# Kernel tuning notes

Measured on AMD Instinct MI355X. Metric: run time of the kernel, lower is better.

## Reference

```python
import jax, jax.numpy as jnp
import numpy as np

N = 50000   # nodes
E = 600000  # edges
H = 128     # hidden_dim


def _linear_params(key, fan_in, fan_out):
    kw, kb = jax.random.split(key)
    s = 1.0 / np.sqrt(fan_in)
    w = jax.random.uniform(kw, (fan_in, fan_out), minval=-s, maxval=s, dtype=jnp.float32)
    b = jax.random.uniform(kb, (fan_out,), minval=-s, maxval=s, dtype=jnp.float32)
    return w, b


def setup_inputs():
    key = jax.random.key(0)
    ks = jax.random.split(key, 9)
    x = jax.random.uniform(ks[0], (N, 1), dtype=jnp.float32)
    pre_h = jax.random.normal(ks[1], (N, H), dtype=jnp.float32)
    edge_index = jax.random.randint(ks[2], (2, E), 0, N, dtype=jnp.int32)
    edge_attr = jax.random.uniform(ks[3], (E, 1), dtype=jnp.float32)
    enc_w, enc_b = _linear_params(ks[4], 1 + H, H)      # BFS_Encoder.linear
    M_w, M_b = _linear_params(ks[5], H + H + 1, H)      # MPNN_Processor.M
    U_w, U_b = _linear_params(ks[6], H + H, H)          # MPNN_Processor.U
    dec_w, dec_b = _linear_params(ks[7], H + H, 1)      # BFS_Decoder.linear
    ter_w, ter_b = _linear_params(ks[8], H + H, 1)      # BFS_Terminator.linear
    return {"x": x, "pre_h": pre_h, "edge_attr": edge_attr,
            "enc_w": enc_w, "enc_b": enc_b, "M_w": M_w, "M_b": M_b,
            "U_w": U_w, "U_b": U_b, "dec_w": dec_w, "dec_b": dec_b,
            "ter_w": ter_w, "ter_b": ter_b, "edge_index": edge_index}


def reference(x, pre_h, edge_attr, enc_w, enc_b, M_w, M_b, U_w, U_b,
              dec_w, dec_b, ter_w, ter_b, edge_index):
    # Encoder: z = relu(Linear([x, pre_h]))
    z = jax.nn.relu(jnp.concatenate([x, pre_h], axis=-1) @ enc_w + enc_b)  # [N,H]

    # Processor (PyG MessagePassing, flow source_to_target):
    # z_i = z[edge_index[1]] (target), z_j = z[edge_index[0]] (source)
    src, tgt = edge_index[0], edge_index[1]
    m = jax.nn.relu(
        jnp.concatenate([z[tgt], z[src], edge_attr], axis=-1) @ M_w + M_b)  # [E,H]
    # scatter-max aggregate into target nodes; empty segments -> 0
    agg = jax.ops.segment_max(m, tgt, num_segments=N)
    agg = jnp.where(jnp.isfinite(agg), agg, 0.0)
    h = jax.nn.relu(jnp.concatenate([z, agg], axis=-1) @ U_w + U_b)  # [N,H]

    # Decoder
    y = jax.nn.sigmoid(jnp.concatenate([z, h], axis=-1) @ dec_w + dec_b)  # [N,1]

    # Terminator: mean over nodes, broadcast-concat, scalar mean
    h_mean = jnp.broadcast_to(jnp.mean(h, axis=0), h.shape)
    ter = jnp.mean(jnp.concatenate([h, h_mean], axis=-1) @ ter_w + ter_b)
    return h, y, ter
```

## Files before the change

### kernel.cpp

```cpp
#include <hip/hip_runtime.h>
#include <hip/hip_bf16.h>
#include <math.h>

#define HD 128
#define APAD 136

typedef short bf16x8 __attribute__((ext_vector_type(8)));
typedef float f32x4 __attribute__((ext_vector_type(4)));

static __device__ __forceinline__ unsigned short f2bf(float f) {
  __hip_bfloat16 b = __float2bfloat16(f);
  return *(unsigned short*)&b;
}
static __device__ __forceinline__ float bflo(unsigned int u) {
  return __uint_as_float(u << 16);
}
static __device__ __forceinline__ float bfhi(unsigned int u) {
  return __uint_as_float(u & 0xffff0000u);
}

__global__ __launch_bounds__(256) void k_frag_hist(
    const float* __restrict__ enc_w, const float* __restrict__ M_w,
    const float* __restrict__ U_w,
    unsigned short* __restrict__ encf, unsigned short* __restrict__ Pf,
    unsigned short* __restrict__ Qf, unsigned short* __restrict__ Uf,
    const int* __restrict__ ei, int* __restrict__ cnt, int E) {
  const int b = blockIdx.x;
  if (b >= 40) {
    const int e = (b - 40) * 256 + threadIdx.x;
    if (e < E) atomicAdd(&cnt[ei[E + e]], 1);
    return;
  }
  const float* W; unsigned short* F; int KS; int lb;
  if (b < 8)       { W = enc_w + HD;     F = encf; KS = 4; lb = b; }
  else if (b < 16) { W = M_w;            F = Pf;   KS = 4; lb = b - 8; }
  else if (b < 24) { W = M_w + HD * HD;  F = Qf;   KS = 4; lb = b - 16; }
  else             { W = U_w;            F = Uf;   KS = 8; lb = b - 24; }
  const int gid = lb * 256 + threadIdx.x;
  const int lane = gid & 63;
  const int ks = (gid >> 6) % KS;
  const int tile = gid / (64 * KS);
  const int col = tile * 16 + (lane & 15);
  const int k0 = ks * 32 + (lane >> 4) * 8;
  unsigned short v[8];
#pragma unroll
  for (int j = 0; j < 8; ++j) v[j] = f2bf(W[(size_t)(k0 + j) * HD + col]);
  unsigned short* dst = F + ((size_t)(tile * KS + ks) * 64 + lane) * 8;
#pragma unroll
  for (int j = 0; j < 8; ++j) dst[j] = v[j];
}

__global__ __launch_bounds__(256) void k_scan_block(
    const int* __restrict__ cnt, int* __restrict__ row_ptr,
    int* __restrict__ partials, int N) {
  __shared__ int s[256];
  const int t = threadIdx.x;
  const int base = blockIdx.x * 1024 + t * 4;
  int v[4], sum = 0;
#pragma unroll
  for (int i = 0; i < 4; ++i) {
    v[i] = (base + i < N) ? cnt[base + i] : 0;
    sum += v[i];
  }
  s[t] = sum;
  __syncthreads();
  for (int off = 1; off < 256; off <<= 1) {
    int xv = (t >= off) ? s[t - off] : 0;
    __syncthreads();
    if (t >= off) s[t] += xv;
    __syncthreads();
  }
  int run = s[t] - sum;
  if (t == 255) partials[blockIdx.x] = s[255];
#pragma unroll
  for (int i = 0; i < 4; ++i) {
    if (base + i < N) row_ptr[base + i] = run;
    run += v[i];
  }
}

__global__ void k_scan_partials(int* __restrict__ partials, int nb) {
  if (threadIdx.x == 0) {
    int run = 0;
    for (int i = 0; i < nb; ++i) { int v = partials[i]; partials[i] = run; run += v; }
  }
}

__global__ __launch_bounds__(256) void k_scan_add(
    int* __restrict__ row_ptr, const int* __restrict__ partials,
    int* __restrict__ cursor, int N) {
  const int base = blockIdx.x * 1024 + threadIdx.x * 4;
  const int p = partials[blockIdx.x];
#pragma unroll
  for (int i = 0; i < 4; ++i) {
    if (base + i < N) {
      int v = row_ptr[base + i] + p;
      row_ptr[base + i] = v;
      cursor[base + i] = v;
    }
  }
}

__global__ __launch_bounds__(256) void k_scatter(
    const int* __restrict__ ei, const float* __restrict__ edge_attr,
    int* __restrict__ cursor, int2* __restrict__ epack, int E) {
  const int e = blockIdx.x * 256 + threadIdx.x;
  if (e >= E) return;
  const int tgt = ei[E + e];
  const int pos = atomicAdd(&cursor[tgt], 1);
  epack[pos] = make_int2(ei[e], __float_as_int(edge_attr[e]));
}

__global__ __launch_bounds__(256, 4) void k_enc_pq(
    const float* __restrict__ x, const float* __restrict__ pre_h,
    const float* __restrict__ enc_w, const float* __restrict__ enc_b,
    const float* __restrict__ M_b,
    const unsigned short* __restrict__ encf, const unsigned short* __restrict__ Pf,
    const unsigned short* __restrict__ Qf,
    unsigned short* __restrict__ zg, unsigned short* __restrict__ Pg,
    unsigned short* __restrict__ Qg) {
  __shared__ unsigned short phs[16 * APAD];
  __shared__ unsigned short zsh[16 * APAD];
  __shared__ float xs[16];
  const int t = threadIdx.x;
  const int n0 = blockIdx.x * 16;

  {
    const int r = t >> 4, c0 = (t & 15) * 8;
    const float4 a = *(const float4*)&pre_h[(size_t)(n0 + r) * HD + c0];
    const float4 b = *(const float4*)&pre_h[(size_t)(n0 + r) * HD + c0 + 4];
    unsigned short* d = &phs[r * APAD + c0];
    d[0] = f2bf(a.x); d[1] = f2bf(a.y); d[2] = f2bf(a.z); d[3] = f2bf(a.w);
    d[4] = f2bf(b.x); d[5] = f2bf(b.y); d[6] = f2bf(b.z); d[7] = f2bf(b.w);
  }
  if (t < 16) xs[t] = x[n0 + t];
  __syncthreads();

  const int w = t >> 6, l = t & 63;
  const int m = l & 15, q = l >> 4;

  bf16x8 af[4];
#pragma unroll
  for (int ks = 0; ks < 4; ++ks)
    af[ks] = *(const bf16x8*)&phs[m * APAD + ks * 32 + q * 8];
  f32x4 acc[2] = {{0, 0, 0, 0}, {0, 0, 0, 0}};
#pragma unroll
  for (int tt = 0; tt < 2; ++tt) {
    const int tn = 2 * w + tt;
#pragma unroll
    for (int ks = 0; ks < 4; ++ks) {
      const bf16x8 bf = *(const bf16x8*)&encf[((size_t)(tn * 4 + ks) * 64 + l) * 8];
      acc[tt] = __builtin_amdgcn_mfma_f32_16x16x32_bf16(af[ks], bf, acc[tt], 0, 0, 0);
    }
  }
#pragma unroll
  for (int tt = 0; tt < 2; ++tt) {
    const int col = (2 * w + tt) * 16 + m;
    const float bb = enc_b[col];
    const float w0 = enc_w[col];
#pragma unroll
    for (int r = 0; r < 4; ++r) {
      const int row = q * 4 + r;
      const float zv = fmaxf(acc[tt][r] + bb + xs[row] * w0, 0.0f);
      zsh[row * APAD + col] = f2bf(zv);
    }
  }
  __syncthreads();

  bf16x8 az[4];
#pragma unroll
  for (int ks = 0; ks < 4; ++ks)
    az[ks] = *(const bf16x8*)&zsh[m * APAD + ks * 32 + q * 8];
  {
    const int r = t >> 4, c0 = (t & 15) * 8;
    *(uint4*)&zg[(size_t)(n0 + r) * HD + c0] = *(const uint4*)&zsh[r * APAD + c0];
  }
  __syncthreads();

  f32x4 pacc[2] = {{0, 0, 0, 0}, {0, 0, 0, 0}};
  f32x4 qacc[2] = {{0, 0, 0, 0}, {0, 0, 0, 0}};
#pragma unroll
  for (int tt = 0; tt < 2; ++tt) {
    const int tn = 2 * w + tt;
#pragma unroll
    for (int ks = 0; ks < 4; ++ks) {
      const bf16x8 bp = *(const bf16x8*)&Pf[((size_t)(tn * 4 + ks) * 64 + l) * 8];
      const bf16x8 bq = *(const bf16x8*)&Qf[((size_t)(tn * 4 + ks) * 64 + l) * 8];
      pacc[tt] = __builtin_amdgcn_mfma_f32_16x16x32_bf16(az[ks], bp, pacc[tt], 0, 0, 0);
      qacc[tt] = __builtin_amdgcn_mfma_f32_16x16x32_bf16(az[ks], bq, qacc[tt], 0, 0, 0);
    }
  }
#pragma unroll
  for (int tt = 0; tt < 2; ++tt) {
    const int col = (2 * w + tt) * 16 + m;
    const float mb = M_b[col];
#pragma unroll
    for (int r = 0; r < 4; ++r) {
      const int row = q * 4 + r;
      phs[row * APAD + col] = f2bf(pacc[tt][r] + mb);
      zsh[row * APAD + col] = f2bf(qacc[tt][r]);
    }
  }
  __syncthreads();
  {
    const int r = t >> 4, c0 = (t & 15) * 8;
    *(uint4*)&Pg[(size_t)(n0 + r) * HD + c0] = *(const uint4*)&phs[r * APAD + c0];
    *(uint4*)&Qg[(size_t)(n0 + r) * HD + c0] = *(const uint4*)&zsh[r * APAD + c0];
  }
}

__global__ __launch_bounds__(256, 6) void k_gather(
    const unsigned short* __restrict__ Pg, const unsigned short* __restrict__ Qg,
    const float* __restrict__ w_attr,
    const int* __restrict__ row_ptr, const int* __restrict__ row_end,
    const int2* __restrict__ epack,
    unsigned short* __restrict__ ag, int N) {
  const int t = threadIdx.x;
  const int w = t >> 6, l = t & 63;
  const int g = l >> 4, j = l & 15;
  const int n0 = blockIdx.x * 32;

  float wv[8];
  {
    const float4 wa = *(const float4*)&w_attr[j * 8];
    const float4 wb = *(const float4*)&w_attr[j * 8 + 4];
    wv[0] = wa.x; wv[1] = wa.y; wv[2] = wa.z; wv[3] = wa.w;
    wv[4] = wb.x; wv[5] = wb.y; wv[6] = wb.z; wv[7] = wb.w;
  }

#pragma unroll
  for (int i = 0; i < 2; ++i) {
    const int r = w * 8 + g * 2 + i;
    const int n = n0 + r;
    const int nc = min(n, N - 1);
    const int rs = row_ptr[nc], re = row_end[nc];
    float acc[8];
#pragma unroll
    for (int c = 0; c < 8; ++c) acc[c] = -INFINITY;
    for (int e = rs; e < re; e += 4) {
      int2 pk[4];
#pragma unroll
      for (int u = 0; u < 4; ++u) pk[u] = epack[min(e + u, re - 1)];
      uint4 qv[4];
#pragma unroll
      for (int u = 0; u < 4; ++u)
        qv[u] = *(const uint4*)&Qg[(size_t)pk[u].x * HD + j * 8];
#pragma unroll
      for (int u = 0; u < 4; ++u) {
        const float a = __int_as_float(pk[u].y);
        const unsigned int qq[4] = {qv[u].x, qv[u].y, qv[u].z, qv[u].w};
#pragma unroll
        for (int c = 0; c < 4; ++c) {
          acc[2 * c]     = fmaxf(acc[2 * c],     fmaf(a, wv[2 * c],     bflo(qq[c])));
          acc[2 * c + 1] = fmaxf(acc[2 * c + 1], fmaf(a, wv[2 * c + 1], bfhi(qq[c])));
        }
      }
    }
    if (n < N) {
      float res[8];
      if (re > rs) {
        const uint4 pv = *(const uint4*)&Pg[(size_t)n * HD + j * 8];
        const unsigned int pp[4] = {pv.x, pv.y, pv.z, pv.w};
#pragma unroll
        for (int c = 0; c < 4; ++c) {
          res[2 * c]     = fmaxf(bflo(pp[c]) + acc[2 * c],     0.0f);
          res[2 * c + 1] = fmaxf(bfhi(pp[c]) + acc[2 * c + 1], 0.0f);
        }
      } else {
#pragma unroll
        for (int c = 0; c < 8; ++c) res[c] = 0.0f;
      }
      uint4 st;
      st.x = (unsigned)f2bf(res[0]) | ((unsigned)f2bf(res[1]) << 16);
      st.y = (unsigned)f2bf(res[2]) | ((unsigned)f2bf(res[3]) << 16);
      st.z = (unsigned)f2bf(res[4]) | ((unsigned)f2bf(res[5]) << 16);
      st.w = (unsigned)f2bf(res[6]) | ((unsigned)f2bf(res[7]) << 16);
      *(uint4*)&ag[(size_t)n * HD + j * 8] = st;
    }
  }
}

__global__ __launch_bounds__(256, 4) void k_update(
    const unsigned short* __restrict__ zg, const unsigned short* __restrict__ ag,
    const unsigned short* __restrict__ Uf,
    const float* __restrict__ U_b, const float* __restrict__ dec_w,
    const float* __restrict__ dec_b,
    float* __restrict__ h_out, float* __restrict__ y_out,
    float* __restrict__ hsum, int N) {
  __shared__ unsigned short zsh[32 * APAD];
  __shared__ unsigned short ash[32 * APAD];
  __shared__ float hcol[HD];
  __shared__ float dacc[32];
  __shared__ float pr[32][8];
  const int t = threadIdx.x;
  const int n0 = blockIdx.x * 32;

  {
    const int r = t >> 3, c0 = (t & 7) * 16;
    const int n = min(n0 + r, N - 1);
    *(uint4*)&zsh[r * APAD + c0]     = *(const uint4*)&zg[(size_t)n * HD + c0];
    *(uint4*)&zsh[r * APAD + c0 + 8] = *(const uint4*)&zg[(size_t)n * HD + c0 + 8];
    *(uint4*)&ash[r * APAD + c0]     = *(const uint4*)&ag[(size_t)n * HD + c0];
    *(uint4*)&ash[r * APAD + c0 + 8] = *(const uint4*)&ag[(size_t)n * HD + c0 + 8];
  }
  if (t < 32) dacc[t] = 0.0f;
  if (t < HD) hcol[t] = 0.0f;
  __syncthreads();

  const int w = t >> 6, l = t & 63;

  const int mt = w & 1, nh = w >> 1;
  const int m = mt * 16 + (l & 15), q = l >> 4;
  bf16x8 afz[4], afa[4];
#pragma unroll
  for (int ks = 0; ks < 4; ++ks) {
    afz[ks] = *(const bf16x8*)&zsh[m * APAD + ks * 32 + q * 8];
    afa[ks] = *(const bf16x8*)&ash[m * APAD + ks * 32 + q * 8];
  }
  f32x4 acc4[4] = {{0, 0, 0, 0}, {0, 0, 0, 0}, {0, 0, 0, 0}, {0, 0, 0, 0}};
#pragma unroll
  for (int tt = 0; tt < 4; ++tt) {
    const int tn = nh * 4 + tt;
#pragma unroll
    for (int ks = 0; ks < 8; ++ks) {
      const bf16x8 bf = *(const bf16x8*)&Uf[((size_t)(tn * 8 + ks) * 64 + l) * 8];
      const bf16x8 a = (ks < 4) ? afz[ks] : afa[ks - 4];
      acc4[tt] = __builtin_amdgcn_mfma_f32_16x16x32_bf16(a, bf, acc4[tt], 0, 0, 0);
    }
  }
  float dp[4] = {0.0f, 0.0f, 0.0f, 0.0f};
#pragma unroll
  for (int tt = 0; tt < 4; ++tt) {
    const int col = (nh * 4 + tt) * 16 + (l & 15);
    const float ub = U_b[col];
    const float dw = dec_w[HD + col];
    float s4 = 0.0f;
#pragma unroll
    for (int r = 0; r < 4; ++r) {
      const int rowl = mt * 16 + q * 4 + r;
      const int n = n0 + rowl;
      float hv = fmaxf(acc4[tt][r] + ub, 0.0f);
      if (n < N) h_out[(size_t)n * HD + col] = hv; else hv = 0.0f;
      s4 += hv;
      dp[r] += hv * dw;
    }
    atomicAdd(&hcol[col], s4);
  }
#pragma unroll
  for (int off = 1; off < 16; off <<= 1) {
#pragma unroll
    for (int r = 0; r < 4; ++r) dp[r] += __shfl_xor(dp[r], off);
  }
  if ((l & 15) == 0) {
#pragma unroll
    for (int r = 0; r < 4; ++r) atomicAdd(&dacc[mt * 16 + q * 4 + r], dp[r]);
  }

  {
    const int r2 = t >> 3, s = t & 7;
    float part = 0.0f;
#pragma unroll
    for (int c = 0; c < 8; ++c) {
      const int kk = s * 16 + 2 * c;
      const unsigned int zu = *(const unsigned int*)&zsh[r2 * APAD + kk];
      part += bflo(zu) * dec_w[kk] + bfhi(zu) * dec_w[kk + 1];
    }
    pr[r2][s] = part;
  }
  __syncthreads();

  if (t < HD) atomicAdd(&hsum[t], hcol[t]);
  if (t < 32 && n0 + t < N) {
    float d = dec_b[0] + dacc[t];
#pragma unroll
    for (int s = 0; s < 8; ++s) d += pr[t][s];
    y_out[n0 + t] = 1.0f / (1.0f + expf(-d));
  }
}

__global__ __launch_bounds__(128) void k_ter(
    const float* __restrict__ hsum, const float* __restrict__ ter_w,
    const float* __restrict__ ter_b, float* __restrict__ out, float invN) {
  __shared__ float r2[2];
  const int t = threadIdx.x;
  float v = (hsum[t] * invN) * (ter_w[t] + ter_w[HD + t]);
#pragma unroll
  for (int o = 32; o > 0; o >>= 1) v += __shfl_down(v, o);
  if ((t & 63) == 0) r2[t >> 6] = v;
  __syncthreads();
  if (t == 0) out[0] = r2[0] + r2[1] + ter_b[0];
}

extern "C" void kernel_launch(void* const* d_in, const int* in_sizes, int n_in,
                              void* d_out, int out_size, void* d_ws, size_t ws_size,
                              hipStream_t stream) {
  const float* x        = (const float*)d_in[0];
  const float* pre_h    = (const float*)d_in[1];
  const float* edge_attr= (const float*)d_in[2];
  const float* enc_w    = (const float*)d_in[3];
  const float* enc_b    = (const float*)d_in[4];
  const float* M_w      = (const float*)d_in[5];
  const float* M_b      = (const float*)d_in[6];
  const float* U_w      = (const float*)d_in[7];
  const float* U_b      = (const float*)d_in[8];
  const float* dec_w    = (const float*)d_in[9];
  const float* dec_b    = (const float*)d_in[10];
  const float* ter_w    = (const float*)d_in[11];
  const float* ter_b    = (const float*)d_in[12];
  const int*   edge_idx = (const int*)d_in[13];

  const int N = in_sizes[0];
  const int E = in_sizes[2];
  const size_t NH = (size_t)N * HD;

  float* out = (float*)d_out;
  float* h_out = out;
  float* y_out = out + NH;
  float* ter_out = out + NH + N;

  unsigned short* zg = (unsigned short*)d_ws;
  unsigned short* Pg = zg + NH;
  unsigned short* Qg = Pg + NH;
  unsigned short* ag = Qg + NH;
  int*   cursor   = (int*)(ag + NH);
  int*   row_ptr  = cursor + N;
  int*   partials = row_ptr + N;
  float* hsum     = (float*)(partials + 64);
  int2*  epack    = (int2*)(hsum + HD);
  unsigned short* encf = (unsigned short*)(epack + E);
  unsigned short* Pf   = encf + 8 * 4 * 64 * 8;
  unsigned short* Qf   = Pf + 8 * 4 * 64 * 8;
  unsigned short* Uf   = Qf + 8 * 4 * 64 * 8;

  hipMemsetAsync(cursor, 0, (2 * (size_t)N + 64 + HD) * sizeof(int), stream);

  const int scan_blocks = (N + 1023) / 1024;
  const int eb = (E + 255) / 256;

  k_frag_hist<<<40 + eb, 256, 0, stream>>>(enc_w, M_w, U_w, encf, Pf, Qf, Uf,
                                           edge_idx, cursor, E);
  k_scan_block<<<scan_blocks, 256, 0, stream>>>(cursor, row_ptr, partials, N);
  k_scan_partials<<<1, 64, 0, stream>>>(partials, scan_blocks);
  k_scan_add<<<scan_blocks, 256, 0, stream>>>(row_ptr, partials, cursor, N);
  k_scatter<<<eb, 256, 0, stream>>>(edge_idx, edge_attr, cursor, epack, E);

  k_enc_pq<<<N / 16, 256, 0, stream>>>(x, pre_h, enc_w, enc_b, M_b,
                                       encf, Pf, Qf, zg, Pg, Qg);
  k_gather<<<(N + 31) / 32, 256, 0, stream>>>(
      Pg, Qg, M_w + 256 * HD, row_ptr, cursor, epack, ag, N);
  k_update<<<(N + 31) / 32, 256, 0, stream>>>(
      zg, ag, Uf, U_b, dec_w, dec_b, h_out, y_out, hsum, N);
  k_ter<<<1, 128, 0, stream>>>(hsum, ter_w, ter_b, ter_out, 1.0f / (float)N);
}
```

Baseline: 274.0 us.

## Fuse all stages into one persistent cooperative kernel with grid syncs

Replaces the chain of separate launches (weight fragment conversion, histogram, three-kernel scan, scatter, encoder, gather, update, terminator) with one cooperative persistent kernel that separates phases with grid.sync. It also fuses gather and update so the aggregated rows stay in shared memory instead of round-tripping through global memory. The column sums are now written per tile and reduced in a later phase instead of using global atomics. The aim is to remove launch gaps and the aggregate buffer traffic. In exchange, occupancy is capped by the cooperative grid size and every phase waits on grid-wide barriers.

After: 705.2 us. 2.57x slower.

```diff
diff --git a/kernel.cpp b/kernel.cpp
--- a/kernel.cpp
+++ b/kernel.cpp
@@ -1,4 +1,5 @@
 #include <hip/hip_runtime.h>
+#include <hip/hip_cooperative_groups.h>
 #include <hip/hip_bf16.h>
 #include <math.h>
 
@@ -7,6 +8,8 @@
 
 typedef short bf16x8 __attribute__((ext_vector_type(8)));
 typedef float f32x4 __attribute__((ext_vector_type(4)));
+
+namespace cg = cooperative_groups;
 
 static __device__ __forceinline__ unsigned short f2bf(float f) {
   __hip_bfloat16 b = __float2bfloat16(f);
@@ -19,376 +22,379 @@
   return __uint_as_float(u & 0xffff0000u);
 }
 
-__global__ __launch_bounds__(256) void k_frag_hist(
-    const float* __restrict__ enc_w, const float* __restrict__ M_w,
-    const float* __restrict__ U_w,
+__global__ __launch_bounds__(256, 4) void k_mega(
+    const float* __restrict__ x, const float* __restrict__ pre_h,
+    const float* __restrict__ edge_attr,
+    const float* __restrict__ enc_w, const float* __restrict__ enc_b,
+    const float* __restrict__ M_w, const float* __restrict__ M_b,
+    const float* __restrict__ U_w, const float* __restrict__ U_b,
+    const float* __restrict__ dec_w, const float* __restrict__ dec_b,
+    const float* __restrict__ ter_w, const float* __restrict__ ter_b,
+    const int* __restrict__ ei,
+    unsigned short* __restrict__ zg, unsigned short* __restrict__ Pg,
+    unsigned short* __restrict__ Qg,
+    int* __restrict__ cursor, int* __restrict__ row_ptr,
+    int* __restrict__ partials, float* __restrict__ hsum,
+    int2* __restrict__ epack,
     unsigned short* __restrict__ encf, unsigned short* __restrict__ Pf,
     unsigned short* __restrict__ Qf, unsigned short* __restrict__ Uf,
-    const int* __restrict__ ei, int* __restrict__ cnt, int E) {
-  const int b = blockIdx.x;
-  if (b >= 40) {
-    const int e = (b - 40) * 256 + threadIdx.x;
-    if (e < E) atomicAdd(&cnt[ei[E + e]], 1);
-    return;
-  }
-  const float* W; unsigned short* F; int KS; int lb;
-  if (b < 8)       { W = enc_w + HD;     F = encf; KS = 4; lb = b; }
-  else if (b < 16) { W = M_w;            F = Pf;   KS = 4; lb = b - 8; }
-  else if (b < 24) { W = M_w + HD * HD;  F = Qf;   KS = 4; lb = b - 16; }
-  else             { W = U_w;            F = Uf;   KS = 8; lb = b - 24; }
-  const int gid = lb * 256 + threadIdx.x;
-  const int lane = gid & 63;
-  const int ks = (gid >> 6) % KS;
-  const int tile = gid / (64 * KS);
-  const int col = tile * 16 + (lane & 15);
-  const int k0 = ks * 32 + (lane >> 4) * 8;
-  unsigned short v[8];
-#pragma unroll
-  for (int j = 0; j < 8; ++j) v[j] = f2bf(W[(size_t)(k0 + j) * HD + col]);
-  unsigned short* dst = F + ((size_t)(tile * KS + ks) * 64 + lane) * 8;
-#pragma unroll
-  for (int j = 0; j < 8; ++j) dst[j] = v[j];
-}
-
-__global__ __launch_bounds__(256) void k_scan_block(
-    const int* __restrict__ cnt, int* __restrict__ row_ptr,
-    int* __restrict__ partials, int N) {
-  __shared__ int s[256];
+    float* __restrict__ hpart,
+    float* __restrict__ h_out, float* __restrict__ y_out,
+    float* __restrict__ ter_out,
+    int N, int E) {
+  cg::grid_group grid = cg::this_grid();
   const int t = threadIdx.x;
-  const int base = blockIdx.x * 1024 + t * 4;
-  int v[4], sum = 0;
-#pragma unroll
-  for (int i = 0; i < 4; ++i) {
-    v[i] = (base + i < N) ? cnt[base + i] : 0;
-    sum += v[i];
-  }
-  s[t] = sum;
-  __syncthreads();
-  for (int off = 1; off < 256; off <<= 1) {
-    int xv = (t >= off) ? s[t - off] : 0;
-    __syncthreads();
-    if (t >= off) s[t] += xv;
-    __syncthreads();
-  }
-  int run = s[t] - sum;
-  if (t == 255) partials[blockIdx.x] = s[255];
-#pragma unroll
-  for (int i = 0; i < 4; ++i) {
-    if (base + i < N) row_ptr[base + i] = run;
-    run += v[i];
-  }
-}
-
-__global__ void k_scan_partials(int* __restrict__ partials, int nb) {
-  if (threadIdx.x == 0) {
-    int run = 0;
-    for (int i = 0; i < nb; ++i) { int v = partials[i]; partials[i] = run; run += v; }
-  }
-}
-
-__global__ __launch_bounds__(256) void k_scan_add(
-    int* __restrict__ row_ptr, const int* __restrict__ partials,
-    int* __restrict__ cursor, int N) {
-  const int base = blockIdx.x * 1024 + threadIdx.x * 4;
-  const int p = partials[blockIdx.x];
-#pragma unroll
-  for (int i = 0; i < 4; ++i) {
-    if (base + i < N) {
-      int v = row_ptr[base + i] + p;
-      row_ptr[base + i] = v;
-      cursor[base + i] = v;
-    }
-  }
-}
-
-__global__ __launch_bounds__(256) void k_scatter(
-    const int* __restrict__ ei, const float* __restrict__ edge_attr,
-    int* __restrict__ cursor, int2* __restrict__ epack, int E) {
-  const int e = blockIdx.x * 256 + threadIdx.x;
-  if (e >= E) return;
-  const int tgt = ei[E + e];
-  const int pos = atomicAdd(&cursor[tgt], 1);
-  epack[pos] = make_int2(ei[e], __float_as_int(edge_attr[e]));
-}
-
-__global__ __launch_bounds__(256, 4) void k_enc_pq(
-    const float* __restrict__ x, const float* __restrict__ pre_h,
-    const float* __restrict__ enc_w, const float* __restrict__ enc_b,
-    const float* __restrict__ M_b,
-    const unsigned short* __restrict__ encf, const unsigned short* __restrict__ Pf,
-    const unsigned short* __restrict__ Qf,
-    unsigned short* __restrict__ zg, unsigned short* __restrict__ Pg,
-    unsigned short* __restrict__ Qg) {
-  __shared__ unsigned short phs[16 * APAD];
-  __shared__ unsigned short zsh[16 * APAD];
-  __shared__ float xs[16];
-  const int t = threadIdx.x;
-  const int n0 = blockIdx.x * 16;
-
-  {
-    const int r = t >> 4, c0 = (t & 15) * 8;
-    const float4 a = *(const float4*)&pre_h[(size_t)(n0 + r) * HD + c0];
-    const float4 b = *(const float4*)&pre_h[(size_t)(n0 + r) * HD + c0 + 4];
-    unsigned short* d = &phs[r * APAD + c0];
-    d[0] = f2bf(a.x); d[1] = f2bf(a.y); d[2] = f2bf(a.z); d[3] = f2bf(a.w);
-    d[4] = f2bf(b.x); d[5] = f2bf(b.y); d[6] = f2bf(b.z); d[7] = f2bf(b.w);
-  }
-  if (t < 16) xs[t] = x[n0 + t];
-  __syncthreads();
-
-  const int w = t >> 6, l = t & 63;
-  const int m = l & 15, q = l >> 4;
-
-  bf16x8 af[4];
-#pragma unroll
-  for (int ks = 0; ks < 4; ++ks)
-    af[ks] = *(const bf16x8*)&phs[m * APAD + ks * 32 + q * 8];
-  f32x4 acc[2] = {{0, 0, 0, 0}, {0, 0, 0, 0}};
-#pragma unroll
-  for (int tt = 0; tt < 2; ++tt) {
-    const int tn = 2 * w + tt;
-#pragma unroll
-    for (int ks = 0; ks < 4; ++ks) {
-      const bf16x8 bf = *(const bf16x8*)&encf[((size_t)(tn * 4 + ks) * 64 + l) * 8];
-      acc[tt] = __builtin_amdgcn_mfma_f32_16x16x32_bf16(af[ks], bf, acc[tt], 0, 0, 0);
-    }
-  }
-#pragma unroll
-  for (int tt = 0; tt < 2; ++tt) {
-    const int col = (2 * w + tt) * 16 + m;
-    const float bb = enc_b[col];
-    const float w0 = enc_w[col];
-#pragma unroll
-    for (int r = 0; r < 4; ++r) {
-      const int row = q * 4 + r;
-      const float zv = fmaxf(acc[tt][r] + bb + xs[row] * w0, 0.0f);
-      zsh[row * APAD + col] = f2bf(zv);
-    }
-  }
-  __syncthreads();
-
-  bf16x8 az[4];
-#pragma unroll
-  for (int ks = 0; ks < 4; ++ks)
-    az[ks] = *(const bf16x8*)&zsh[m * APAD + ks * 32 + q * 8];
-  {
-    const int r = t >> 4, c0 = (t & 15) * 8;
-    *(uint4*)&zg[(size_t)(n0 + r) * HD + c0] = *(const uint4*)&zsh[r * APAD + c0];
-  }
-  __syncthreads();
-
-  f32x4 pacc[2] = {{0, 0, 0, 0}, {0, 0, 0, 0}};
-  f32x4 qacc[2] = {{0, 0, 0, 0}, {0, 0, 0, 0}};
-#pragma unroll
-  for (int tt = 0; tt < 2; ++tt) {
-    const int tn = 2 * w + tt;
-#pragma unroll
-    for (int ks = 0; ks < 4; ++ks) {
-      const bf16x8 bp = *(const bf16x8*)&Pf[((size_t)(tn * 4 + ks) * 64 + l) * 8];
-      const bf16x8 bq = *(const bf16x8*)&Qf[((size_t)(tn * 4 + ks) * 64 + l) * 8];
-      pacc[tt] = __builtin_amdgcn_mfma_f32_16x16x32_bf16(az[ks], bp, pacc[tt], 0, 0, 0);
-      qacc[tt] = __builtin_amdgcn_mfma_f32_16x16x32_bf16(az[ks], bq, qacc[tt], 0, 0, 0);
-    }
-  }
-#pragma unroll
-  for (int tt = 0; tt < 2; ++tt) {
-    const int col = (2 * w + tt) * 16 + m;
-    const float mb = M_b[col];
-#pragma unroll
-    for (int r = 0; r < 4; ++r) {
-      const int row = q * 4 + r;
-      phs[row * APAD + col] = f2bf(pacc[tt][r] + mb);
-      zsh[row * APAD + col] = f2bf(qacc[tt][r]);
-    }
-  }
-  __syncthreads();
-  {
-    const int r = t >> 4, c0 = (t & 15) * 8;
-    *(uint4*)&Pg[(size_t)(n0 + r) * HD + c0] = *(const uint4*)&phs[r * APAD + c0];
-    *(uint4*)&Qg[(size_t)(n0 + r) * HD + c0] = *(const uint4*)&zsh[r * APAD + c0];
-  }
-}
-
-__global__ __launch_bounds__(256, 6) void k_gather(
-    const unsigned short* __restrict__ Pg, const unsigned short* __restrict__ Qg,
-    const float* __restrict__ w_attr,
-    const int* __restrict__ row_ptr, const int* __restrict__ row_end,
-    const int2* __restrict__ epack,
-    unsigned short* __restrict__ ag, int N) {
-  const int t = threadIdx.x;
-  const int w = t >> 6, l = t & 63;
-  const int g = l >> 4, j = l & 15;
-  const int n0 = blockIdx.x * 32;
-
-  float wv[8];
-  {
-    const float4 wa = *(const float4*)&w_attr[j * 8];
-    const float4 wb = *(const float4*)&w_attr[j * 8 + 4];
-    wv[0] = wa.x; wv[1] = wa.y; wv[2] = wa.z; wv[3] = wa.w;
-    wv[4] = wb.x; wv[5] = wb.y; wv[6] = wb.z; wv[7] = wb.w;
-  }
-
-#pragma unroll
-  for (int i = 0; i < 2; ++i) {
-    const int r = w * 8 + g * 2 + i;
-    const int n = n0 + r;
-    const int nc = min(n, N - 1);
-    const int rs = row_ptr[nc], re = row_end[nc];
-    float acc[8];
-#pragma unroll
-    for (int c = 0; c < 8; ++c) acc[c] = -INFINITY;
-    for (int e = rs; e < re; e += 4) {
-      int2 pk[4];
-#pragma unroll
-      for (int u = 0; u < 4; ++u) pk[u] = epack[min(e + u, re - 1)];
-      uint4 qv[4];
-#pragma unroll
-      for (int u = 0; u < 4; ++u)
-        qv[u] = *(const uint4*)&Qg[(size_t)pk[u].x * HD + j * 8];
-#pragma unroll
-      for (int u = 0; u < 4; ++u) {
-        const float a = __int_as_float(pk[u].y);
-        const unsigned int qq[4] = {qv[u].x, qv[u].y, qv[u].z, qv[u].w};
-#pragma unroll
-        for (int c = 0; c < 4; ++c) {
-          acc[2 * c]     = fmaxf(acc[2 * c],     fmaf(a, wv[2 * c],     bflo(qq[c])));
-          acc[2 * c + 1] = fmaxf(acc[2 * c + 1], fmaf(a, wv[2 * c + 1], bfhi(qq[c])));
-        }
-      }
-    }
-    if (n < N) {
-      float res[8];
-      if (re > rs) {
-        const uint4 pv = *(const uint4*)&Pg[(size_t)n * HD + j * 8];
-        const unsigned int pp[4] = {pv.x, pv.y, pv.z, pv.w};
-#pragma unroll
-        for (int c = 0; c < 4; ++c) {
-          res[2 * c]     = fmaxf(bflo(pp[c]) + acc[2 * c],     0.0f);
-          res[2 * c + 1] = fmaxf(bfhi(pp[c]) + acc[2 * c + 1], 0.0f);
-        }
-      } else {
-#pragma unroll
-        for (int c = 0; c < 8; ++c) res[c] = 0.0f;
-      }
-      uint4 st;
-      st.x = (unsigned)f2bf(res[0]) | ((unsigned)f2bf(res[1]) << 16);
-      st.y = (unsigned)f2bf(res[2]) | ((unsigned)f2bf(res[3]) << 16);
-      st.z = (unsigned)f2bf(res[4]) | ((unsigned)f2bf(res[5]) << 16);
-      st.w = (unsigned)f2bf(res[6]) | ((unsigned)f2bf(res[7]) << 16);
-      *(uint4*)&ag[(size_t)n * HD + j * 8] = st;
-    }
-  }
-}
-
-__global__ __launch_bounds__(256, 4) void k_update(
-    const unsigned short* __restrict__ zg, const unsigned short* __restrict__ ag,
-    const unsigned short* __restrict__ Uf,
-    const float* __restrict__ U_b, const float* __restrict__ dec_w,
-    const float* __restrict__ dec_b,
-    float* __restrict__ h_out, float* __restrict__ y_out,
-    float* __restrict__ hsum, int N) {
+  const int bi = blockIdx.x;
+  const int nb = gridDim.x;
+  const int gt = bi * 256 + t;
+  const int nthr = nb * 256;
+
   __shared__ unsigned short zsh[32 * APAD];
   __shared__ unsigned short ash[32 * APAD];
   __shared__ float hcol[HD];
   __shared__ float dacc[32];
   __shared__ float pr[32][8];
-  const int t = threadIdx.x;
-  const int n0 = blockIdx.x * 32;
-
+  __shared__ int si[256];
+  __shared__ float xs[16];
+  __shared__ int poff_sh;
+
+  if (bi < 40) {
+    const int b = bi;
+    const float* W; unsigned short* F; int KS; int lb;
+    if (b < 8)       { W = enc_w + HD;     F = encf; KS = 4; lb = b; }
+    else if (b < 16) { W = M_w;            F = Pf;   KS = 4; lb = b - 8; }
+    else if (b < 24) { W = M_w + HD * HD;  F = Qf;   KS = 4; lb = b - 16; }
+    else             { W = U_w;            F = Uf;   KS = 8; lb = b - 24; }
+    const int gid = lb * 256 + t;
+    const int lane = gid & 63;
+    const int ks = (gid >> 6) % KS;
+    const int tile = gid / (64 * KS);
+    const int col = tile * 16 + (lane & 15);
+    const int k0 = ks * 32 + (lane >> 4) * 8;
+    unsigned short v[8];
+#pragma unroll
+    for (int j = 0; j < 8; ++j) v[j] = f2bf(W[(size_t)(k0 + j) * HD + col]);
+    unsigned short* dst = F + ((size_t)(tile * KS + ks) * 64 + lane) * 8;
+#pragma unroll
+    for (int j = 0; j < 8; ++j) dst[j] = v[j];
+  }
+  for (int i = gt; i < N; i += nthr) cursor[i] = 0;
+  if (gt < HD) hsum[gt] = 0.0f;
+  grid.sync();
+
+  for (int e = gt; e < E; e += nthr) atomicAdd(&cursor[ei[E + e]], 1);
+  grid.sync();
+
+  const int scan_blocks = (N + 1023) >> 10;
+  if (bi < scan_blocks) {
+    const int base = bi * 1024 + t * 4;
+    int v[4], sum = 0;
+#pragma unroll
+    for (int i = 0; i < 4; ++i) {
+      v[i] = (base + i < N) ? cursor[base + i] : 0;
+      sum += v[i];
+    }
+    si[t] = sum;
+    __syncthreads();
+    for (int off = 1; off < 256; off <<= 1) {
+      int xv = (t >= off) ? si[t - off] : 0;
+      __syncthreads();
+      if (t >= off) si[t] += xv;
+      __syncthreads();
+    }
+    int run = si[t] - sum;
+    if (t == 255) partials[bi] = si[255];
+#pragma unroll
+    for (int i = 0; i < 4; ++i) {
+      if (base + i < N) row_ptr[base + i] = run;
+      run += v[i];
+    }
+  }
+  grid.sync();
+
+  if (bi < scan_blocks) {
+    if (t < 64) {
+      int v = (t < bi) ? partials[t] : 0;
+#pragma unroll
+      for (int o = 32; o > 0; o >>= 1) v += __shfl_down(v, o);
+      if (t == 0) poff_sh = v;
+    }
+    __syncthreads();
+    const int p = poff_sh;
+    const int base = bi * 1024 + t * 4;
+#pragma unroll
+    for (int i = 0; i < 4; ++i) {
+      if (base + i < N) {
+        int v2 = row_ptr[base + i] + p;
+        row_ptr[base + i] = v2;
+        cursor[base + i] = v2;
+      }
+    }
+  }
+  grid.sync();
+
+  for (int e = gt; e < E; e += nthr) {
+    const int tgt = ei[E + e];
+    const int pos = atomicAdd(&cursor[tgt], 1);
+    epack[pos] = make_int2(ei[e], __float_as_int(edge_attr[e]));
+  }
   {
-    const int r = t >> 3, c0 = (t & 7) * 16;
-    const int n = min(n0 + r, N - 1);
-    *(uint4*)&zsh[r * APAD + c0]     = *(const uint4*)&zg[(size_t)n * HD + c0];
-    *(uint4*)&zsh[r * APAD + c0 + 8] = *(const uint4*)&zg[(size_t)n * HD + c0 + 8];
-    *(uint4*)&ash[r * APAD + c0]     = *(const uint4*)&ag[(size_t)n * HD + c0];
-    *(uint4*)&ash[r * APAD + c0 + 8] = *(const uint4*)&ag[(size_t)n * HD + c0 + 8];
-  }
-  if (t < 32) dacc[t] = 0.0f;
-  if (t < HD) hcol[t] = 0.0f;
-  __syncthreads();
-
-  const int w = t >> 6, l = t & 63;
-
-  const int mt = w & 1, nh = w >> 1;
-  const int m = mt * 16 + (l & 15), q = l >> 4;
-  bf16x8 afz[4], afa[4];
-#pragma unroll
-  for (int ks = 0; ks < 4; ++ks) {
-    afz[ks] = *(const bf16x8*)&zsh[m * APAD + ks * 32 + q * 8];
-    afa[ks] = *(const bf16x8*)&ash[m * APAD + ks * 32 + q * 8];
-  }
-  f32x4 acc4[4] = {{0, 0, 0, 0}, {0, 0, 0, 0}, {0, 0, 0, 0}, {0, 0, 0, 0}};
-#pragma unroll
-  for (int tt = 0; tt < 4; ++tt) {
-    const int tn = nh * 4 + tt;
-#pragma unroll
-    for (int ks = 0; ks < 8; ++ks) {
-      const bf16x8 bf = *(const bf16x8*)&Uf[((size_t)(tn * 8 + ks) * 64 + l) * 8];
-      const bf16x8 a = (ks < 4) ? afz[ks] : afa[ks - 4];
-      acc4[tt] = __builtin_amdgcn_mfma_f32_16x16x32_bf16(a, bf, acc4[tt], 0, 0, 0);
-    }
-  }
-  float dp[4] = {0.0f, 0.0f, 0.0f, 0.0f};
-#pragma unroll
-  for (int tt = 0; tt < 4; ++tt) {
-    const int col = (nh * 4 + tt) * 16 + (l & 15);
-    const float ub = U_b[col];
-    const float dw = dec_w[HD + col];
-    float s4 = 0.0f;
-#pragma unroll
-    for (int r = 0; r < 4; ++r) {
-      const int rowl = mt * 16 + q * 4 + r;
-      const int n = n0 + rowl;
-      float hv = fmaxf(acc4[tt][r] + ub, 0.0f);
-      if (n < N) h_out[(size_t)n * HD + col] = hv; else hv = 0.0f;
-      s4 += hv;
-      dp[r] += hv * dw;
-    }
-    atomicAdd(&hcol[col], s4);
-  }
-#pragma unroll
-  for (int off = 1; off < 16; off <<= 1) {
-#pragma unroll
-    for (int r = 0; r < 4; ++r) dp[r] += __shfl_xor(dp[r], off);
-  }
-  if ((l & 15) == 0) {
-#pragma unroll
-    for (int r = 0; r < 4; ++r) atomicAdd(&dacc[mt * 16 + q * 4 + r], dp[r]);
-  }
+    const int ntiles16 = N >> 4;
+    const int w = t >> 6, l = t & 63;
+    const int m = l & 15, q = l >> 4;
+    for (int vb = bi; vb < ntiles16; vb += nb) {
+      const int n0 = vb << 4;
+      __syncthreads();
+      {
+        const int r = t >> 4, c0 = (t & 15) * 8;
+        const float4 a = *(const float4*)&pre_h[(size_t)(n0 + r) * HD + c0];
+        const float4 b2 = *(const float4*)&pre_h[(size_t)(n0 + r) * HD + c0 + 4];
+        unsigned short* d = &ash[r * APAD + c0];
+        d[0] = f2bf(a.x); d[1] = f2bf(a.y); d[2] = f2bf(a.z); d[3] = f2bf(a.w);
+        d[4] = f2bf(b2.x); d[5] = f2bf(b2.y); d[6] = f2bf(b2.z); d[7] = f2bf(b2.w);
+      }
+      if (t < 16) xs[t] = x[n0 + t];
+      __syncthreads();
+
+      bf16x8 af[4];
+#pragma unroll
+      for (int ks = 0; ks < 4; ++ks)
+        af[ks] = *(const bf16x8*)&ash[m * APAD + ks * 32 + q * 8];
+      f32x4 acc[2] = {{0, 0, 0, 0}, {0, 0, 0, 0}};
+#pragma unroll
+      for (int tt = 0; tt < 2; ++tt) {
+        const int tn = 2 * w + tt;
+#pragma unroll
+        for (int ks = 0; ks < 4; ++ks) {
+          const bf16x8 bf = *(const bf16x8*)&encf[((size_t)(tn * 4 + ks) * 64 + l) * 8];
+          acc[tt] = __builtin_amdgcn_mfma_f32_16x16x32_bf16(af[ks], bf, acc[tt], 0, 0, 0);
+        }
+      }
+#pragma unroll
+      for (int tt = 0; tt < 2; ++tt) {
+        const int col = (2 * w + tt) * 16 + m;
+        const float bb = enc_b[col];
+        const float w0 = enc_w[col];
+#pragma unroll
+        for (int r = 0; r < 4; ++r) {
+          const int row = q * 4 + r;
+          const float zv = fmaxf(acc[tt][r] + bb + xs[row] * w0, 0.0f);
+          zsh[row * APAD + col] = f2bf(zv);
+        }
+      }
+      __syncthreads();
+
+      bf16x8 az[4];
+#pragma unroll
+      for (int ks = 0; ks < 4; ++ks)
+        az[ks] = *(const bf16x8*)&zsh[m * APAD + ks * 32 + q * 8];
+      {
+        const int r = t >> 4, c0 = (t & 15) * 8;
+        *(uint4*)&zg[(size_t)(n0 + r) * HD + c0] = *(const uint4*)&zsh[r * APAD + c0];
+      }
+      __syncthreads();
+
+      f32x4 pacc[2] = {{0, 0, 0, 0}, {0, 0, 0, 0}};
+      f32x4 qacc[2] = {{0, 0, 0, 0}, {0, 0, 0, 0}};
+#pragma unroll
+      for (int tt = 0; tt < 2; ++tt) {
+        const int tn = 2 * w + tt;
+#pragma unroll
+        for (int ks = 0; ks < 4; ++ks) {
+          const bf16x8 bp = *(const bf16x8*)&Pf[((size_t)(tn * 4 + ks) * 64 + l) * 8];
+          const bf16x8 bq = *(const bf16x8*)&Qf[((size_t)(tn * 4 + ks) * 64 + l) * 8];
+          pacc[tt] = __builtin_amdgcn_mfma_f32_16x16x32_bf16(az[ks], bp, pacc[tt], 0, 0, 0);
+          qacc[tt] = __builtin_amdgcn_mfma_f32_16x16x32_bf16(az[ks], bq, qacc[tt], 0, 0, 0);
+        }
+      }
+#pragma unroll
+      for (int tt = 0; tt < 2; ++tt) {
+        const int col = (2 * w + tt) * 16 + m;
+        const float mb = M_b[col];
+#pragma unroll
+        for (int r = 0; r < 4; ++r) {
+          const int row = q * 4 + r;
+          ash[row * APAD + col] = f2bf(pacc[tt][r] + mb);
+          zsh[row * APAD + col] = f2bf(qacc[tt][r]);
+        }
+      }
+      __syncthreads();
+      {
+        const int r = t >> 4, c0 = (t & 15) * 8;
+        *(uint4*)&Pg[(size_t)(n0 + r) * HD + c0] = *(const uint4*)&ash[r * APAD + c0];
+        *(uint4*)&Qg[(size_t)(n0 + r) * HD + c0] = *(const uint4*)&zsh[r * APAD + c0];
+      }
+    }
+  }
+  grid.sync();
 
   {
-    const int r2 = t >> 3, s = t & 7;
-    float part = 0.0f;
-#pragma unroll
-    for (int c = 0; c < 8; ++c) {
-      const int kk = s * 16 + 2 * c;
-      const unsigned int zu = *(const unsigned int*)&zsh[r2 * APAD + kk];
-      part += bflo(zu) * dec_w[kk] + bfhi(zu) * dec_w[kk + 1];
-    }
-    pr[r2][s] = part;
-  }
-  __syncthreads();
-
-  if (t < HD) atomicAdd(&hsum[t], hcol[t]);
-  if (t < 32 && n0 + t < N) {
-    float d = dec_b[0] + dacc[t];
-#pragma unroll
-    for (int s = 0; s < 8; ++s) d += pr[t][s];
-    y_out[n0 + t] = 1.0f / (1.0f + expf(-d));
-  }
-}
-
-__global__ __launch_bounds__(128) void k_ter(
-    const float* __restrict__ hsum, const float* __restrict__ ter_w,
-    const float* __restrict__ ter_b, float* __restrict__ out, float invN) {
-  __shared__ float r2[2];
-  const int t = threadIdx.x;
-  float v = (hsum[t] * invN) * (ter_w[t] + ter_w[HD + t]);
-#pragma unroll
-  for (int o = 32; o > 0; o >>= 1) v += __shfl_down(v, o);
-  if ((t & 63) == 0) r2[t >> 6] = v;
-  __syncthreads();
-  if (t == 0) out[0] = r2[0] + r2[1] + ter_b[0];
+    const int w = t >> 6, l = t & 63;
+    const int g = l >> 4, j = l & 15;
+    const float* w_attr = M_w + 256 * HD;
+    float wv[8];
+    {
+      const float4 wa = *(const float4*)&w_attr[j * 8];
+      const float4 wb = *(const float4*)&w_attr[j * 8 + 4];
+      wv[0] = wa.x; wv[1] = wa.y; wv[2] = wa.z; wv[3] = wa.w;
+      wv[4] = wb.x; wv[5] = wb.y; wv[6] = wb.z; wv[7] = wb.w;
+    }
+    const int ntiles32 = (N + 31) >> 5;
+    for (int vb = bi; vb < ntiles32; vb += nb) {
+      const int n0 = vb << 5;
+      __syncthreads();
+      {
+        const int r = t >> 3, c0 = (t & 7) * 16;
+        const int n = min(n0 + r, N - 1);
+        *(uint4*)&zsh[r * APAD + c0]     = *(const uint4*)&zg[(size_t)n * HD + c0];
+        *(uint4*)&zsh[r * APAD + c0 + 8] = *(const uint4*)&zg[(size_t)n * HD + c0 + 8];
+      }
+      if (t < 32) dacc[t] = 0.0f;
+      if (t < HD) hcol[t] = 0.0f;
+
+#pragma unroll
+      for (int i = 0; i < 2; ++i) {
+        const int r = w * 8 + g * 2 + i;
+        const int n = n0 + r;
+        const int nc = min(n, N - 1);
+        const int rs = row_ptr[nc], re = cursor[nc];
+        float acc[8];
+#pragma unroll
+        for (int c = 0; c < 8; ++c) acc[c] = -INFINITY;
+        for (int e = rs; e < re; e += 4) {
+          int2 pk[4];
+#pragma unroll
+          for (int u = 0; u < 4; ++u) pk[u] = epack[min(e + u, re - 1)];
+          uint4 qv[4];
+#pragma unroll
+          for (int u = 0; u < 4; ++u)
+            qv[u] = *(const uint4*)&Qg[(size_t)pk[u].x * HD + j * 8];
+#pragma unroll
+          for (int u = 0; u < 4; ++u) {
+            const float a = __int_as_float(pk[u].y);
+            const unsigned int qq[4] = {qv[u].x, qv[u].y, qv[u].z, qv[u].w};
+#pragma unroll
+            for (int c = 0; c < 4; ++c) {
+              acc[2 * c]     = fmaxf(acc[2 * c],     fmaf(a, wv[2 * c],     bflo(qq[c])));
+              acc[2 * c + 1] = fmaxf(acc[2 * c + 1], fmaf(a, wv[2 * c + 1], bfhi(qq[c])));
+            }
+          }
+        }
+        float res[8];
+        if (n < N && re > rs) {
+          const uint4 pv = *(const uint4*)&Pg[(size_t)n * HD + j * 8];
+          const unsigned int pp[4] = {pv.x, pv.y, pv.z, pv.w};
+#pragma unroll
+          for (int c = 0; c < 4; ++c) {
+            res[2 * c]     = fmaxf(bflo(pp[c]) + acc[2 * c],     0.0f);
+            res[2 * c + 1] = fmaxf(bfhi(pp[c]) + acc[2 * c + 1], 0.0f);
+          }
+        } else {
+#pragma unroll
+          for (int c = 0; c < 8; ++c) res[c] = 0.0f;
+        }
+        uint4 st;
+        st.x = (unsigned)f2bf(res[0]) | ((unsigned)f2bf(res[1]) << 16);
+        st.y = (unsigned)f2bf(res[2]) | ((unsigned)f2bf(res[3]) << 16);
+        st.z = (unsigned)f2bf(res[4]) | ((unsigned)f2bf(res[5]) << 16);
+        st.w = (unsigned)f2bf(res[6]) | ((unsigned)f2bf(res[7]) << 16);
+        *(uint4*)&ash[r * APAD + j * 8] = st;
+      }
+      __syncthreads();
+
+      const int mt = w & 1, nh = w >> 1;
+      const int m = mt * 16 + (l & 15), q = l >> 4;
+      bf16x8 afz[4], afa[4];
+#pragma unroll
+      for (int ks = 0; ks < 4; ++ks) {
+        afz[ks] = *(const bf16x8*)&zsh[m * APAD + ks * 32 + q * 8];
+        afa[ks] = *(const bf16x8*)&ash[m * APAD + ks * 32 + q * 8];
+      }
+      f32x4 acc4[4] = {{0, 0, 0, 0}, {0, 0, 0, 0}, {0, 0, 0, 0}, {0, 0, 0, 0}};
+#pragma unroll
+      for (int tt = 0; tt < 4; ++tt) {
+        const int tn = nh * 4 + tt;
+#pragma unroll
+        for (int ks = 0; ks < 8; ++ks) {
+          const bf16x8 bf = *(const bf16x8*)&Uf[((size_t)(tn * 8 + ks) * 64 + l) * 8];
+          const bf16x8 a = (ks < 4) ? afz[ks] : afa[ks - 4];
+          acc4[tt] = __builtin_amdgcn_mfma_f32_16x16x32_bf16(a, bf, acc4[tt], 0, 0, 0);
+        }
+      }
+      float dp[4] = {0.0f, 0.0f, 0.0f, 0.0f};
+#pragma unroll
+      for (int tt = 0; tt < 4; ++tt) {
+        const int col = (nh * 4 + tt) * 16 + (l & 15);
+        const float ub = U_b[col];
+        const float dw = dec_w[HD + col];
+        float s4 = 0.0f;
+#pragma unroll
+        for (int r = 0; r < 4; ++r) {
+          const int rowl = mt * 16 + q * 4 + r;
+          const int n = n0 + rowl;
+          float hv = fmaxf(acc4[tt][r] + ub, 0.0f);
+          if (n < N) h_out[(size_t)n * HD + col] = hv; else hv = 0.0f;
+          s4 += hv;
+          dp[r] += hv * dw;
+        }
+        atomicAdd(&hcol[col], s4);
+      }
+#pragma unroll
+      for (int off = 1; off < 16; off <<= 1) {
+#pragma unroll
+        for (int r = 0; r < 4; ++r) dp[r] += __shfl_xor(dp[r], off);
+      }
+      if ((l & 15) == 0) {
+#pragma unroll
+        for (int r = 0; r < 4; ++r) atomicAdd(&dacc[mt * 16 + q * 4 + r], dp[r]);
+      }
+      {
+        const int r2 = t >> 3, s = t & 7;
+        float part = 0.0f;
+#pragma unroll
+        for (int c = 0; c < 8; ++c) {
+          const int kk = s * 16 + 2 * c;
+          const unsigned int zu = *(const unsigned int*)&zsh[r2 * APAD + kk];
+          part += bflo(zu) * dec_w[kk] + bfhi(zu) * dec_w[kk + 1];
+        }
+        pr[r2][s] = part;
+      }
+      __syncthreads();
+
+      if (t < HD) hpart[(size_t)vb * HD + t] = hcol[t];
+      if (t < 32 && n0 + t < N) {
+        float d = dec_b[0] + dacc[t];
+#pragma unroll
+        for (int s = 0; s < 8; ++s) d += pr[t][s];
+        y_out[n0 + t] = 1.0f / (1.0f + expf(-d));
+      }
+    }
+  }
+  grid.sync();
+
+  if (bi < 64) {
+    const int NB = (N + 31) >> 5;
+    const int col = t & (HD - 1);
+    const int half = t >> 7;
+    float acc = 0.0f;
+    for (int r = bi * 2 + half; r < NB; r += 128)
+      acc += hpart[(size_t)r * HD + col];
+    if (half) hcol[col] = acc;
+    __syncthreads();
+    if (!half) atomicAdd(&hsum[col], acc + hcol[col]);
+  }
+  grid.sync();
+
+  if (bi == 0) {
+    const float invN = 1.0f / (float)N;
+    float v = 0.0f;
+    if (t < HD) v = (hsum[t] * invN) * (ter_w[t] + ter_w[HD + t]);
+#pragma unroll
+    for (int o = 32; o > 0; o >>= 1) v += __shfl_down(v, o);
+    if (t < HD && (t & 63) == 0) dacc[t >> 6] = v;
+    __syncthreads();
+    if (t == 0) ter_out[0] = dacc[0] + dacc[1] + ter_b[0];
+  }
 }
 
 extern "C" void kernel_launch(void* const* d_in, const int* in_sizes, int n_in,
@@ -409,8 +415,8 @@
   const float* ter_b    = (const float*)d_in[12];
   const int*   edge_idx = (const int*)d_in[13];
 
-  const int N = in_sizes[0];
-  const int E = in_sizes[2];
+  int N = in_sizes[0];
+  int E = in_sizes[2];
   const size_t NH = (size_t)N * HD;
 
   float* out = (float*)d_out;
@@ -431,24 +437,31 @@
   unsigned short* Pf   = encf + 8 * 4 * 64 * 8;
   unsigned short* Qf   = Pf + 8 * 4 * 64 * 8;
   unsigned short* Uf   = Qf + 8 * 4 * 64 * 8;
-
-  hipMemsetAsync(cursor, 0, (2 * (size_t)N + 64 + HD) * sizeof(int), stream);
-
-  const int scan_blocks = (N + 1023) / 1024;
-  const int eb = (E + 255) / 256;
-
-  k_frag_hist<<<40 + eb, 256, 0, stream>>>(enc_w, M_w, U_w, encf, Pf, Qf, Uf,
-                                           edge_idx, cursor, E);
-  k_scan_block<<<scan_blocks, 256, 0, stream>>>(cursor, row_ptr, partials, N);
-  k_scan_partials<<<1, 64, 0, stream>>>(partials, scan_blocks);
-  k_scan_add<<<scan_blocks, 256, 0, stream>>>(row_ptr, partials, cursor, N);
-  k_scatter<<<eb, 256, 0, stream>>>(edge_idx, edge_attr, cursor, epack, E);
-
-  k_enc_pq<<<N / 16, 256, 0, stream>>>(x, pre_h, enc_w, enc_b, M_b,
-                                       encf, Pf, Qf, zg, Pg, Qg);
-  k_gather<<<(N + 31) / 32, 256, 0, stream>>>(
-      Pg, Qg, M_w + 256 * HD, row_ptr, cursor, epack, ag, N);
-  k_update<<<(N + 31) / 32, 256, 0, stream>>>(
-      zg, ag, Uf, U_b, dec_w, dec_b, h_out, y_out, hsum, N);
-  k_ter<<<1, 128, 0, stream>>>(hsum, ter_w, ter_b, ter_out, 1.0f / (float)N);
+  float* hpart = (float*)(Uf + 16 * 256 * 8);
+
+  int dev = 0;
+  hipGetDevice(&dev);
+  int numCU = 0;
+  hipDeviceGetAttribute(&numCU, hipDeviceAttributeMultiprocessorCount, dev);
+  if (numCU <= 0) numCU = 256;
+  int bpc = 0;
+  hipOccupancyMaxActiveBlocksPerMultiprocessor(
+      &bpc, reinterpret_cast<const void*>(k_mega), 256, 0);
+  if (bpc < 1) bpc = 1;
+  long grid = (long)numCU * (long)bpc;
+  if (grid > 3125) grid = 3125;
+
+  void* args[] = {
+      (void*)&x, (void*)&pre_h, (void*)&edge_attr,
+      (void*)&enc_w, (void*)&enc_b, (void*)&M_w, (void*)&M_b,
+      (void*)&U_w, (void*)&U_b, (void*)&dec_w, (void*)&dec_b,
+      (void*)&ter_w, (void*)&ter_b, (void*)&edge_idx,
+      (void*)&zg, (void*)&Pg, (void*)&Qg,
+      (void*)&cursor, (void*)&row_ptr, (void*)&partials, (void*)&hsum,
+      (void*)&epack, (void*)&encf, (void*)&Pf, (void*)&Qf, (void*)&Uf,
+      (void*)&hpart, (void*)&h_out, (void*)&y_out, (void*)&ter_out,
+      (void*)&N, (void*)&E};
+
+  hipLaunchCooperativeKernel(reinterpret_cast<const void*>(k_mega),
+                             dim3((unsigned)grid), dim3(256), args, 0, stream);
 }
```
